# Kernel tuning notes

Hardware: AMD Instinct MI355X
Metric: run time of the kernel (lower is better)

The kernel has to match this reference:

```python
import jax, jax.numpy as jnp
import numpy as np
import math

B, CIN, H, W = 4, 256, 64, 64
COUT = 64
K = 7  # out_kernel


def setup_inputs() -> dict:
    key = jax.random.key(0)
    ks = jax.random.split(key, 9)
    s = 0.05
    x = jax.random.normal(ks[0], (B, CIN, H, W), dtype=jnp.float32)
    Wq = jax.random.normal(ks[1], (COUT, CIN), dtype=jnp.float32) * s
    bq = jax.random.normal(ks[2], (COUT,), dtype=jnp.float32) * s
    Wk = jax.random.normal(ks[3], (COUT, CIN), dtype=jnp.float32) * s
    bk = jax.random.normal(ks[4], (COUT,), dtype=jnp.float32) * s
    Wv = jax.random.normal(ks[5], (COUT, CIN), dtype=jnp.float32) * s
    bv = jax.random.normal(ks[6], (COUT,), dtype=jnp.float32) * s
    Wout = jax.random.normal(ks[7], (COUT, COUT, K, K), dtype=jnp.float32) * s
    bout = jax.random.normal(ks[8], (COUT,), dtype=jnp.float32) * s
    return {"x": x, "Wq": Wq, "bq": bq, "Wk": Wk, "bk": bk,
            "Wv": Wv, "bv": bv, "Wout": Wout, "bout": bout}


def reference(x, Wq, bq, Wk, bk, Wv, bv, Wout, bout):
    b, c, h, w = x.shape
    C = Wq.shape[0]
    hw = h * w
    # 1x1 convs -> (b, h, w, C) channels-last
    qs = jnp.einsum('bchw,oc->bhwo', x, Wq) + bq
    ksp = jnp.einsum('bchw,oc->bhwo', x, Wk) + bk
    vs = jnp.einsum('bchw,oc->bhwo', x, Wv) + bv
    # full QK^T attention over all h*w positions
    qk = jnp.einsum('bic,bjc->bij',
                    qs.reshape(b, hw, C), ksp.reshape(b, hw, C)) / math.sqrt(float(C))
    diag = jnp.arange(hw)
    qk = qk.at[:, diag, diag].set(0.0)  # diagonal zeroed BEFORE softmax
    attn = jax.nn.softmax(qk, axis=-1).reshape(b, h, w, h, w)
    # clamped local-window indices (offsets -K//2 .. K//2)
    off = jnp.arange(K) - K // 2
    idx_h = jnp.clip(jnp.arange(h)[:, None] + off[None, :], 0, h - 1)  # (h,K)
    idx_w = jnp.clip(jnp.arange(w)[:, None] + off[None, :], 0, w - 1)  # (w,K)
    # gather attention weights at local neighborhood: (b,h,w,K,K)
    g = jnp.take_along_axis(attn, idx_h[None, :, None, :, None], axis=3)  # (b,h,w,K,w)
    g = jnp.take_along_axis(g, idx_w[None, None, :, None, :], axis=4)     # (b,h,w,K,K)
    # gather V at local neighborhood: (b,h,w,K,K,C)
    vn = vs[:, idx_h]            # (b,h,K,w,C)
    vn = vn[:, :, :, idx_w]      # (b,h,K,w,K,C)
    vn = jnp.transpose(vn, (0, 1, 3, 2, 4, 5))  # (b,h,w,K,K,C)
    # KxK stride-K conv over the (K,K) window == full contraction per pixel
    out = jnp.einsum('bhwij,bhwijc,ocij->bhwo', g, vn, Wout) + bout
    out = jax.nn.relu(out)
    return jnp.transpose(out, (0, 3, 1, 2))  # (b, C, h, w)
```

## Files before the change

### kernel.cpp

```cpp
#include <hip/hip_runtime.h>
#include <hip/hip_bf16.h>
#include <math.h>

#define BATCH 4
#define CIN   256
#define HH    64
#define WW    64
#define HW    4096
#define COUT  64
#define KK    7
#define NTAP  49
#define NSEG  16

#define QSCALE 0.18033688011112042f
#define C2SCALE 0.18033688011112042f

typedef __attribute__((ext_vector_type(8))) short bf16x8;
typedef __attribute__((ext_vector_type(4))) float f32x4;
typedef __attribute__((ext_vector_type(4))) unsigned short u16x4;

__global__ void prep_kernel(
    const float* __restrict__ Wq, const float* __restrict__ bq,
    const float* __restrict__ Wk, const float* __restrict__ bk,
    const float* __restrict__ Wv, const float* __restrict__ bv,
    const float* __restrict__ Wout,
    __hip_bfloat16* __restrict__ Wb192, float* __restrict__ bias192,
    __hip_bfloat16* __restrict__ W2b)
{
    const int idx = blockIdx.x * 256 + threadIdx.x;
    if (idx < 192 * 256) {
        const int row = idx >> 8, c = idx & 255;
        float wsrc;
        if (row < 64)       wsrc = Wq[row * 256 + c];
        else if (row < 128) wsrc = Wk[(row - 64) * 256 + c];
        else                wsrc = Wv[(row - 128) * 256 + c];
        Wb192[idx] = __float2bfloat16(wsrc);
        if (c == 0) {
            float bsrc;
            if (row < 64)       bsrc = bq[row];
            else if (row < 128) bsrc = bk[row - 64];
            else                bsrc = bv[row - 128];
            bias192[row] = bsrc;
        }
    } else if (idx < 192 * 256 + COUT * NTAP * COUT) {
        const int j = idx - 192 * 256;
        const int o = j / (NTAP * COUT);
        const int r = j - o * (NTAP * COUT);
        const int t = r >> 6;
        const int c = r & 63;
        W2b[j] = __float2bfloat16(Wout[((size_t)o * COUT + c) * NTAP + t]);
    }
}

__global__ __launch_bounds__(256) void qkv_mfma(
    const float* __restrict__ x,
    const __hip_bfloat16* __restrict__ Wb192, const float* __restrict__ bias192,
    float* __restrict__ q, float* __restrict__ k, float* __restrict__ v,
    __hip_bfloat16* __restrict__ qh, __hip_bfloat16* __restrict__ kh)
{
    const int blk = blockIdx.x;
    const int b   = blk >> 8;
    const int p0  = (blk & 255) * 16;
    const int tid = threadIdx.x;
    const int wv  = tid >> 6;
    const int l   = tid & 63;
    const int lg  = l >> 4, lr = l & 15;

    __shared__ __attribute__((aligned(16))) __hip_bfloat16 xsh[16 * 256];

    {
        const int c0 = tid >> 2;
        const int p4 = tid & 3;
        const float4* xb4 = (const float4*)(x + ((size_t)b * CIN) * HW + p0);
#pragma unroll
        for (int it = 0; it < 4; ++it) {
            const int cc = c0 + it * 64;
            const float4 xv = xb4[(size_t)cc * (HW / 4) + p4];
            __hip_bfloat16* dst = &xsh[((cc >> 3) * 16) * 8 + (cc & 7)];
            dst[(p4 * 4 + 0) * 8] = __float2bfloat16(xv.x);
            dst[(p4 * 4 + 1) * 8] = __float2bfloat16(xv.y);
            dst[(p4 * 4 + 2) * 8] = __float2bfloat16(xv.z);
            dst[(p4 * 4 + 3) * 8] = __float2bfloat16(xv.w);
        }
    }
    __syncthreads();

    f32x4 acc0 = {0.f,0.f,0.f,0.f}, acc1 = {0.f,0.f,0.f,0.f}, acc2 = {0.f,0.f,0.f,0.f};
    const short* wb  = (const short*)Wb192;
    const short* xs  = (const short*)xsh;

#pragma unroll
    for (int s = 0; s < 8; ++s) {
        const bf16x8 af = *(const bf16x8*)(xs + (size_t)(((s * 4 + lg) * 16 + lr)) * 8);
        const bf16x8 b0 = *(const bf16x8*)(wb + (size_t)((wv * 3 + 0) * 16 + lr) * 256 + s * 32 + lg * 8);
        const bf16x8 b1 = *(const bf16x8*)(wb + (size_t)((wv * 3 + 1) * 16 + lr) * 256 + s * 32 + lg * 8);
        const bf16x8 b2 = *(const bf16x8*)(wb + (size_t)((wv * 3 + 2) * 16 + lr) * 256 + s * 32 + lg * 8);
        acc0 = __builtin_amdgcn_mfma_f32_16x16x32_bf16(af, b0, acc0, 0, 0, 0);
        acc1 = __builtin_amdgcn_mfma_f32_16x16x32_bf16(af, b1, acc1, 0, 0, 0);
        acc2 = __builtin_amdgcn_mfma_f32_16x16x32_bf16(af, b2, acc2, 0, 0, 0);
    }

    f32x4 accs[3] = {acc0, acc1, acc2};
#pragma unroll
    for (int i = 0; i < 3; ++i) {
        const int otile = wv * 3 + i;
        const int kind  = otile >> 2;
        const int o     = (otile & 3) * 16 + lr;
        const float bias = bias192[otile * 16 + lr];
#pragma unroll
        for (int j = 0; j < 4; ++j) {
            const int p = p0 + lg * 4 + j;
            const size_t addr = ((size_t)b * HW + p) * (size_t)COUT + o;
            const float val = accs[i][j] + bias;
            if (kind == 0)      { q[addr] = val; qh[addr] = __float2bfloat16(val * QSCALE); }
            else if (kind == 1) { k[addr] = val; kh[addr] = __float2bfloat16(val); }
            else                { v[addr] = val; }
        }
    }
}

__global__ __launch_bounds__(256) void qk_stats_mfma(
    const __hip_bfloat16* __restrict__ qh, const __hip_bfloat16* __restrict__ kh,
    float* __restrict__ s_part)
{
    const int blk   = blockIdx.x;
    const int b     = blk >> 8;
    const int panel = (blk >> 4) & 15;
    const int jseg  = blk & 15;
    const int tid   = threadIdx.x;
    const int w     = tid >> 6;
    const int l     = tid & 63;
    const int lg    = l >> 4;
    const int lr    = l & 15;
    const int R0    = panel * 256 + w * 64;

    const short* qb = (const short*)(qh + ((size_t)b * HW) * COUT);
    const short* kb = (const short*)(kh + ((size_t)b * HW) * COUT);

    bf16x8 a[4][2];
#pragma unroll
    for (int rt = 0; rt < 4; ++rt) {
        a[rt][0] = *(const bf16x8*)(qb + (size_t)(R0 + rt * 16 + lr) * COUT + lg * 8);
        a[rt][1] = *(const bf16x8*)(qb + (size_t)(R0 + rt * 16 + lr) * COUT + 32 + lg * 8);
    }

    float s[4][4];
#pragma unroll
    for (int rt = 0; rt < 4; ++rt)
#pragma unroll
        for (int i = 0; i < 4; ++i) s[rt][i] = 0.f;

    const int j0 = jseg * 256;
    const short* kptr = kb + (size_t)(j0 + lr) * COUT + lg * 8;

    bf16x8 p0 = *(const bf16x8*)(kptr);
    bf16x8 p1 = *(const bf16x8*)(kptr + 32);
    kptr += 16 * COUT;

    for (int it = 0; it < 16; ++it) {
        bf16x8 n0, n1;
        if (it != 15) {
            n0 = *(const bf16x8*)(kptr);
            n1 = *(const bf16x8*)(kptr + 32);
            kptr += 16 * COUT;
        }
        const int jb = j0 + it * 16;
#pragma unroll
        for (int rt = 0; rt < 4; ++rt) {
            f32x4 d = {0.f, 0.f, 0.f, 0.f};
            d = __builtin_amdgcn_mfma_f32_16x16x32_bf16(a[rt][0], p0, d, 0, 0, 0);
            d = __builtin_amdgcn_mfma_f32_16x16x32_bf16(a[rt][1], p1, d, 0, 0, 0);
            if (jb == R0 + rt * 16) {
                d.x = (lr == lg * 4 + 0) ? 0.f : d.x;
                d.y = (lr == lg * 4 + 1) ? 0.f : d.y;
                d.z = (lr == lg * 4 + 2) ? 0.f : d.z;
                d.w = (lr == lg * 4 + 3) ? 0.f : d.w;
            }
            s[rt][0] += exp2f(d.x);
            s[rt][1] += exp2f(d.y);
            s[rt][2] += exp2f(d.z);
            s[rt][3] += exp2f(d.w);
        }
        p0 = n0; p1 = n1;
    }

#pragma unroll
    for (int rt = 0; rt < 4; ++rt) {
#pragma unroll
        for (int off = 1; off < 16; off <<= 1) {
            s[rt][0] += __shfl_xor(s[rt][0], off, 64);
            s[rt][1] += __shfl_xor(s[rt][1], off, 64);
            s[rt][2] += __shfl_xor(s[rt][2], off, 64);
            s[rt][3] += __shfl_xor(s[rt][3], off, 64);
        }
        if (lr == 0) {
            float4 res = {s[rt][0], s[rt][1], s[rt][2], s[rt][3]};
            *(float4*)(s_part + (size_t)jseg * (BATCH * HW) + (size_t)b * HW +
                       R0 + rt * 16 + lg * 4) = res;
        }
    }
}

__global__ __launch_bounds__(256) void gcalc_kernel(
    const float* __restrict__ q, const float* __restrict__ k,
    const float* __restrict__ s_part,
    float* __restrict__ g)
{
    const int tid  = threadIdx.x;
    const int pixl = tid >> 6;
    const int t    = tid & 63;
    const int row  = blockIdx.x * 4 + pixl;
    if (t >= NTAP) return;

    const int b  = row >> 12;
    const int pi = row & 4095;
    const int h  = pi >> 6, w = pi & 63;
    const int ti = t / 7, tj = t % 7;
    const int jh = min(max(h + ti - 3, 0), HH - 1);
    const int jw = min(max(w + tj - 3, 0), WW - 1);
    const int jidx = (jh << 6) | jw;

    const float4* qr = (const float4*)(q + (size_t)row * COUT);
    const float4* kr = (const float4*)(k + ((size_t)b * HW + jidx) * COUT);
    float d = 0.f;
#pragma unroll
    for (int i = 0; i < 16; ++i) {
        const float4 a = qr[i], c = kr[i];
        d += a.x * c.x + a.y * c.y + a.z * c.z + a.w * c.w;
    }
    float s = 0.f;
#pragma unroll
    for (int seg = 0; seg < NSEG; ++seg)
        s += s_part[(size_t)seg * (BATCH * HW) + row];
    const float num = (jidx == pi) ? 1.0f : exp2f(d * C2SCALE);
    g[(size_t)row * NTAP + t] = num / s;
}

__global__ __launch_bounds__(256) void out_mfma(
    const float* __restrict__ g, const float* __restrict__ v,
    const __hip_bfloat16* __restrict__ W2b, const float* __restrict__ bout,
    float* __restrict__ out)
{
    const int blk = blockIdx.x;
    const int b   = blk >> 7;
    const int h   = (blk >> 1) & 63;
    const int w0  = (blk & 1) * 32;
    const int tid = threadIdx.x;
    const int wv  = tid >> 6;
    const int l   = tid & 63;
    const int lg  = l >> 4, lr = l & 15;

    __shared__ __attribute__((aligned(16))) __hip_bfloat16 gvsh[2][32][72];
    __shared__ float gsh[32][NTAP];

    const int row0 = b * HW + h * 64 + w0;
    for (int i = tid; i < 32 * NTAP; i += 256) {
        const int w = i / NTAP, t = i - w * NTAP;
        gsh[w][t] = g[(size_t)(row0 + w) * NTAP + t];
    }

    f32x4 acc0 = {0.f, 0.f, 0.f, 0.f};
    f32x4 acc1 = {0.f, 0.f, 0.f, 0.f};
    const float4* vb = (const float4*)(v + ((size_t)b * HW) * COUT);
    const short* wb  = (const short*)W2b + (size_t)(wv * 16 + lr) * (NTAP * COUT);

    const int fw = tid >> 4;
    const int fc4 = tid & 15;

    __syncthreads();

    for (int t = 0; t < NTAP; ++t) {
        const int dh = t / 7 - 3, dw = t - (t / 7) * 7 - 3;
        const int jh = min(max(h + dh, 0), HH - 1);
        __hip_bfloat16* dstbuf = &gvsh[t & 1][0][0];
#pragma unroll
        for (int rep = 0; rep < 2; ++rep) {
            const int w  = fw + rep * 16;
            const int jw = min(max(w0 + w + dw, 0), WW - 1);
            const float4 vvv = vb[(size_t)((jh << 6) + jw) * 16 + fc4];
            const float gg = gsh[w][t];
            u16x4 pk;
            pk.x = __builtin_bit_cast(unsigned short, __float2bfloat16(vvv.x * gg));
            pk.y = __builtin_bit_cast(unsigned short, __float2bfloat16(vvv.y * gg));
            pk.z = __builtin_bit_cast(unsigned short, __float2bfloat16(vvv.z * gg));
            pk.w = __builtin_bit_cast(unsigned short, __float2bfloat16(vvv.w * gg));
            *(u16x4*)(dstbuf + w * 72 + fc4 * 4) = pk;
        }
        const bf16x8 b0 = *(const bf16x8*)(wb + t * 64 + lg * 8);
        const bf16x8 b1 = *(const bf16x8*)(wb + t * 64 + 32 + lg * 8);
        __syncthreads();
        const short* gsrc = (const short*)&gvsh[t & 1][0][0];
        const bf16x8 a00 = *(const bf16x8*)(gsrc + (size_t)lr * 72 + lg * 8);
        const bf16x8 a01 = *(const bf16x8*)(gsrc + (size_t)lr * 72 + 32 + lg * 8);
        const bf16x8 a10 = *(const bf16x8*)(gsrc + (size_t)(16 + lr) * 72 + lg * 8);
        const bf16x8 a11 = *(const bf16x8*)(gsrc + (size_t)(16 + lr) * 72 + 32 + lg * 8);
        acc0 = __builtin_amdgcn_mfma_f32_16x16x32_bf16(a00, b0, acc0, 0, 0, 0);
        acc0 = __builtin_amdgcn_mfma_f32_16x16x32_bf16(a01, b1, acc0, 0, 0, 0);
        acc1 = __builtin_amdgcn_mfma_f32_16x16x32_bf16(a10, b0, acc1, 0, 0, 0);
        acc1 = __builtin_amdgcn_mfma_f32_16x16x32_bf16(a11, b1, acc1, 0, 0, 0);
    }

    const int o  = wv * 16 + lr;
    const float bo = bout[o];
    float* obase = out + ((size_t)(b * COUT + o) * HW) + h * 64 + w0 + lg * 4;
    float4 r0, r1;
    r0.x = fmaxf(acc0.x + bo, 0.f); r0.y = fmaxf(acc0.y + bo, 0.f);
    r0.z = fmaxf(acc0.z + bo, 0.f); r0.w = fmaxf(acc0.w + bo, 0.f);
    r1.x = fmaxf(acc1.x + bo, 0.f); r1.y = fmaxf(acc1.y + bo, 0.f);
    r1.z = fmaxf(acc1.z + bo, 0.f); r1.w = fmaxf(acc1.w + bo, 0.f);
    *(float4*)obase        = r0;
    *(float4*)(obase + 16) = r1;
}

extern "C" void kernel_launch(void* const* d_in, const int* in_sizes, int n_in,
                              void* d_out, int out_size, void* d_ws, size_t ws_size,
                              hipStream_t stream)
{
    const float* x    = (const float*)d_in[0];
    const float* Wq   = (const float*)d_in[1];
    const float* bq   = (const float*)d_in[2];
    const float* Wk   = (const float*)d_in[3];
    const float* bk   = (const float*)d_in[4];
    const float* Wv   = (const float*)d_in[5];
    const float* bv   = (const float*)d_in[6];
    const float* Wout = (const float*)d_in[7];
    const float* bout = (const float*)d_in[8];
    float* out = (float*)d_out;

    float* ws     = (float*)d_ws;
    float* q      = ws;
    float* k      = q + (size_t)BATCH * HW * COUT;
    float* v      = k + (size_t)BATCH * HW * COUT;
    float* s_part = v + (size_t)BATCH * HW * COUT;
    float* g      = s_part + (size_t)NSEG * BATCH * HW;
    float* bias192 = g + (size_t)BATCH * HW * NTAP;
    __hip_bfloat16* qh    = (__hip_bfloat16*)(bias192 + 256);
    __hip_bfloat16* kh    = qh + (size_t)BATCH * HW * COUT;
    __hip_bfloat16* W2b   = kh + (size_t)BATCH * HW * COUT;
    __hip_bfloat16* Wb192 = W2b + (size_t)COUT * NTAP * COUT;

    prep_kernel<<<(192 * 256 + COUT * NTAP * COUT + 255) / 256, 256, 0, stream>>>(
        Wq, bq, Wk, bk, Wv, bv, Wout, Wb192, bias192, W2b);
    qkv_mfma<<<BATCH * (HW / 16), 256, 0, stream>>>(x, Wb192, bias192, q, k, v, qh, kh);
    qk_stats_mfma<<<BATCH * 16 * NSEG, 256, 0, stream>>>(qh, kh, s_part);
    gcalc_kernel<<<BATCH * HW / 4, 256, 0, stream>>>(q, k, s_part, g);
    out_mfma<<<512, 256, 0, stream>>>(g, v, W2b, bout, out);
}
```

Measured before the change: 207.5 us.

## Compute local-window attention logits with MFMA on bf16 q/k rows

Replaces the per-tap scalar fp32 dot-product kernel with an MFMA kernel. For each (batch, row, row-offset) block it computes the 64x64 dot products between a query row and a key row, then gathers the 7 needed column taps from shared memory. This lets the qkv kernel stop writing fp32 q and k, which cuts global writes and later reads. Logits now come from bf16 q/k, matching the softmax-denominator kernel but with lower precision than before. Most of the 64x64 tile is discarded, and each block does far more FLOPs than it needs.

Result: faster. 183.5 us (-11.6%).

```diff
diff --git a/kernel.cpp b/kernel.cpp
--- a/kernel.cpp
+++ b/kernel.cpp
@@ -13,7 +13,6 @@
 #define NSEG  16
 
 #define QSCALE 0.18033688011112042f
-#define C2SCALE 0.18033688011112042f
 
 typedef __attribute__((ext_vector_type(8))) short bf16x8;
 typedef __attribute__((ext_vector_type(4))) float f32x4;
@@ -55,7 +54,7 @@
 __global__ __launch_bounds__(256) void qkv_mfma(
     const float* __restrict__ x,
     const __hip_bfloat16* __restrict__ Wb192, const float* __restrict__ bias192,
-    float* __restrict__ q, float* __restrict__ k, float* __restrict__ v,
+    float* __restrict__ v,
     __hip_bfloat16* __restrict__ qh, __hip_bfloat16* __restrict__ kh)
 {
     const int blk = blockIdx.x;
@@ -112,8 +111,8 @@
             const int p = p0 + lg * 4 + j;
             const size_t addr = ((size_t)b * HW + p) * (size_t)COUT + o;
             const float val = accs[i][j] + bias;
-            if (kind == 0)      { q[addr] = val; qh[addr] = __float2bfloat16(val * QSCALE); }
-            else if (kind == 1) { k[addr] = val; kh[addr] = __float2bfloat16(val); }
+            if (kind == 0)      { qh[addr] = __float2bfloat16(val * QSCALE); }
+            else if (kind == 1) { kh[addr] = __float2bfloat16(val); }
             else                { v[addr] = val; }
         }
     }
@@ -201,39 +200,63 @@
     }
 }
 
-__global__ __launch_bounds__(256) void gcalc_kernel(
-    const float* __restrict__ q, const float* __restrict__ k,
-    const float* __restrict__ s_part,
-    float* __restrict__ g)
-{
-    const int tid  = threadIdx.x;
-    const int pixl = tid >> 6;
-    const int t    = tid & 63;
-    const int row  = blockIdx.x * 4 + pixl;
-    if (t >= NTAP) return;
-
-    const int b  = row >> 12;
-    const int pi = row & 4095;
-    const int h  = pi >> 6, w = pi & 63;
-    const int ti = t / 7, tj = t % 7;
-    const int jh = min(max(h + ti - 3, 0), HH - 1);
-    const int jw = min(max(w + tj - 3, 0), WW - 1);
-    const int jidx = (jh << 6) | jw;
-
-    const float4* qr = (const float4*)(q + (size_t)row * COUT);
-    const float4* kr = (const float4*)(k + ((size_t)b * HW + jidx) * COUT);
-    float d = 0.f;
-#pragma unroll
-    for (int i = 0; i < 16; ++i) {
-        const float4 a = qr[i], c = kr[i];
-        d += a.x * c.x + a.y * c.y + a.z * c.z + a.w * c.w;
-    }
-    float s = 0.f;
-#pragma unroll
-    for (int seg = 0; seg < NSEG; ++seg)
-        s += s_part[(size_t)seg * (BATCH * HW) + row];
-    const float num = (jidx == pi) ? 1.0f : exp2f(d * C2SCALE);
-    g[(size_t)row * NTAP + t] = num / s;
+__global__ __launch_bounds__(256) void gcalc_mfma(
+    const __hip_bfloat16* __restrict__ qh, const __hip_bfloat16* __restrict__ kh,
+    const float* __restrict__ s_part, float* __restrict__ g)
+{
+    const int blk = blockIdx.x;
+    const int dh  = blk % 7;
+    const int bh  = blk / 7;
+    const int h   = bh & 63;
+    const int b   = bh >> 6;
+    const int tid = threadIdx.x;
+    const int wv  = tid >> 6;
+    const int l   = tid & 63;
+    const int lg  = l >> 4, lr = l & 15;
+
+    const int jh = min(max(h + dh - 3, 0), HH - 1);
+
+    __shared__ float Dsh[64][65];
+    __shared__ float rsh[64];
+
+    if (tid < 64) {
+        float s = 0.f;
+        const size_t base = (size_t)b * HW + h * 64 + tid;
+#pragma unroll
+        for (int seg = 0; seg < NSEG; ++seg)
+            s += s_part[(size_t)seg * (BATCH * HW) + base];
+        rsh[tid] = 1.0f / s;
+    }
+
+    const short* qb = (const short*)(qh + ((size_t)b * HW + h * 64) * COUT);
+    const short* kb = (const short*)(kh + ((size_t)b * HW + jh * 64) * COUT);
+
+    const bf16x8 a0 = *(const bf16x8*)(qb + (size_t)(wv * 16 + lr) * COUT + lg * 8);
+    const bf16x8 a1 = *(const bf16x8*)(qb + (size_t)(wv * 16 + lr) * COUT + 32 + lg * 8);
+
+#pragma unroll
+    for (int ct = 0; ct < 4; ++ct) {
+        const bf16x8 b0 = *(const bf16x8*)(kb + (size_t)(ct * 16 + lr) * COUT + lg * 8);
+        const bf16x8 b1 = *(const bf16x8*)(kb + (size_t)(ct * 16 + lr) * COUT + 32 + lg * 8);
+        f32x4 d = {0.f, 0.f, 0.f, 0.f};
+        d = __builtin_amdgcn_mfma_f32_16x16x32_bf16(a0, b0, d, 0, 0, 0);
+        d = __builtin_amdgcn_mfma_f32_16x16x32_bf16(a1, b1, d, 0, 0, 0);
+        const int row = wv * 16 + lg * 4;
+        const int col = ct * 16 + lr;
+        Dsh[row + 0][col] = d.x;
+        Dsh[row + 1][col] = d.y;
+        Dsh[row + 2][col] = d.z;
+        Dsh[row + 3][col] = d.w;
+    }
+    __syncthreads();
+
+    for (int e = tid; e < 64 * 7; e += 256) {
+        const int w  = e / 7;
+        const int tj = e - w * 7;
+        const int jw = min(max(w + tj - 3, 0), WW - 1);
+        const float num = (jh == h && jw == w) ? 1.0f : exp2f(Dsh[w][jw]);
+        g[((size_t)b * HW + h * 64 + w) * NTAP + dh * 7 + tj] = num * rsh[w];
+    }
 }
 
 __global__ __launch_bounds__(256) void out_mfma(
@@ -327,12 +350,10 @@
     const float* bout = (const float*)d_in[8];
     float* out = (float*)d_out;
 
-    float* ws     = (float*)d_ws;
-    float* q      = ws;
-    float* k      = q + (size_t)BATCH * HW * COUT;
-    float* v      = k + (size_t)BATCH * HW * COUT;
-    float* s_part = v + (size_t)BATCH * HW * COUT;
-    float* g      = s_part + (size_t)NSEG * BATCH * HW;
+    float* ws      = (float*)d_ws;
+    float* v       = ws;
+    float* s_part  = v + (size_t)BATCH * HW * COUT;
+    float* g       = s_part + (size_t)NSEG * BATCH * HW;
     float* bias192 = g + (size_t)BATCH * HW * NTAP;
     __hip_bfloat16* qh    = (__hip_bfloat16*)(bias192 + 256);
     __hip_bfloat16* kh    = qh + (size_t)BATCH * HW * COUT;
@@ -341,8 +362,8 @@
 
     prep_kernel<<<(192 * 256 + COUT * NTAP * COUT + 255) / 256, 256, 0, stream>>>(
         Wq, bq, Wk, bk, Wv, bv, Wout, Wb192, bias192, W2b);
-    qkv_mfma<<<BATCH * (HW / 16), 256, 0, stream>>>(x, Wb192, bias192, q, k, v, qh, kh);
+    qkv_mfma<<<BATCH * (HW / 16), 256, 0, stream>>>(x, Wb192, bias192, v, qh, kh);
     qk_stats_mfma<<<BATCH * 16 * NSEG, 256, 0, stream>>>(qh, kh, s_part);
-    gcalc_kernel<<<BATCH * HW / 4, 256, 0, stream>>>(q, k, s_part, g);
+    gcalc_mfma<<<BATCH * HH * 7, 256, 0, stream>>>(qh, kh, s_part, g);
     out_mfma<<<512, 256, 0, stream>>>(g, v, W2b, bout, out);
 }
```
